# Kernel optimization log

Hardware: AMD Instinct MI355X
Metric: run time of the kernel (lower is better)

## Reference

```python
import jax, jax.numpy as jnp
import numpy as np

TEMP = 0.05
MOMENTUM = 0.2
NUM_SAMPLES = 65536
NUM_FEATURES = 256
BATCH = 512
EPS = 1e-12

def _l2norm(x, axis=-1):
    return x / jnp.sqrt(jnp.sum(x * x, axis=axis, keepdims=True) + EPS)

def setup_inputs() -> dict:
    key = jax.random.key(0)
    k1, k2, k3 = jax.random.split(key, 3)
    inputs = _l2norm(jax.random.normal(k1, (BATCH, NUM_FEATURES), dtype=jnp.float32))
    targets = jax.random.randint(k2, (BATCH,), 0, NUM_SAMPLES, dtype=jnp.int32)
    features = _l2norm(jax.random.normal(k3, (NUM_SAMPLES, NUM_FEATURES), dtype=jnp.float32))
    return {"inputs": inputs, "targets": targets, "features": features}

def reference(inputs, targets, features):
    # ClusterMemory forward (mode='CM'): logits = (inputs @ features.T) / temp
    logits = jnp.matmul(inputs, features.T) / TEMP  # [B, num_samples]

    # CM side-effect: sequential per-sample EMA scatter update of the memory bank
    # features[y] = m*features[y] + (1-m)*x; features[y] /= ||features[y]||
    # Order-dependent over the batch (duplicate targets), so use lax.scan.
    def step(feats, xy):
        x, y = xy
        row = MOMENTUM * feats[y] + (1.0 - MOMENTUM) * x
        row = row / jnp.sqrt(jnp.sum(row * row) + EPS)
        return feats.at[y].set(row), None

    new_features, _ = jax.lax.scan(step, features, (inputs, targets))
    return logits, new_features
```

## Files before the change

### kernel.cpp

```cpp
#include <hip/hip_runtime.h>
#include <hip/hip_bf16.h>

#define NSAMP   65536
#define NFEAT   256
#define BATCHSZ 512
#define LOGITS_ELEMS ((size_t)BATCHSZ * NSAMP)

typedef __attribute__((ext_vector_type(4))) float f32x4;
typedef __attribute__((ext_vector_type(8))) short bf16x8;

#define BM 128
#define BN 128
#define BK 64

#define B_HI_OFF ((size_t)0)
#define B_LO_OFF ((size_t)33554432)
#define A_HI_OFF ((size_t)67108864)
#define A_LO_OFF ((size_t)67371008)
#define WS_NEEDED ((size_t)(67371008 + 262144))
#define CHUNK_BYTES 16384

#define FSLOTS (NSAMP * (NFEAT / 8))
#define ASLOTS (BATCHSZ * (NFEAT / 8))

__device__ inline unsigned short bf16_bits(float x) {
  return __builtin_bit_cast(unsigned short, __float2bfloat16(x));
}

#define GLOAD_LDS16(gp, lp)                                         \
  __builtin_amdgcn_global_load_lds(                                 \
      (const __attribute__((address_space(1))) void*)(gp),          \
      (__attribute__((address_space(3))) void*)(lp), 16, 0, 0)

__global__ __launch_bounds__(256)
void cm_pack_kernel(const float* __restrict__ inputs,
                    const float* __restrict__ features,
                    char* __restrict__ ws,
                    float* __restrict__ newF) {
  const int idx = blockIdx.x * 256 + threadIdx.x;
  const float* g;
  size_t dst_hi, dst_lo;
  if (idx < FSLOTS) {
    const int R = idx >> 5, s5 = idx & 31;
    g = features + (size_t)R * NFEAT + s5 * 8;
    const int p = R >> 7, r = R & 127, ks = s5 >> 3, slot = s5 & 7;
    const size_t off = (size_t)(p * 4 + ks) * CHUNK_BYTES +
                       r * 128 + ((slot * 16) ^ ((r & 7) << 4));
    dst_hi = B_HI_OFF + off;
    dst_lo = B_LO_OFF + off;
    float* o = newF + (size_t)R * NFEAT + s5 * 8;
    *(f32x4*)o       = *(const f32x4*)g;
    *(f32x4*)(o + 4) = *(const f32x4*)(g + 4);
  } else if (idx < FSLOTS + ASLOTS) {
    const int j = idx - FSLOTS;
    const int R = j >> 5, s5 = j & 31;
    g = inputs + (size_t)R * NFEAT + s5 * 8;
    const int p = R >> 7, r = R & 127, ks = s5 >> 3, slot = s5 & 7;
    const size_t off = (size_t)(p * 4 + ks) * CHUNK_BYTES +
                       r * 128 + ((slot * 16) ^ ((r & 7) << 4));
    dst_hi = A_HI_OFF + off;
    dst_lo = A_LO_OFF + off;
  } else {
    return;
  }
  f32x4 v0 = *(const f32x4*)g;
  f32x4 v1 = *(const f32x4*)(g + 4);
  bf16x8 hi, lo;
  #pragma unroll
  for (int e = 0; e < 8; ++e) {
    float x = (e < 4) ? v0[e & 3] : v1[e & 3];
    unsigned short h = bf16_bits(x);
    float hf = __bfloat162float(__builtin_bit_cast(__hip_bfloat16, h));
    hi[e] = (short)h;
    lo[e] = (short)bf16_bits(x - hf);
  }
  *(bf16x8*)(ws + dst_hi) = hi;
  *(bf16x8*)(ws + dst_lo) = lo;
}

__device__ __forceinline__ void mfma_block(const char* smem, int lane,
                                           int m_off, int n_off,
                                           f32x4 acc[4][4]) {
  #pragma unroll
  for (int kc = 0; kc < 2; ++kc) {
    const int kbyte = kc * 64 + ((lane >> 4) << 4);
    const int xr    = (lane & 7) << 4;
    bf16x8 ah[4], al[4], bh[4], bl[4];
    #pragma unroll
    for (int m = 0; m < 4; ++m) {
      const int r   = m_off + m * 16 + (lane & 15);
      const int off = r * 128 + (kbyte ^ xr);
      ah[m] = *(const bf16x8*)(smem + off);
      al[m] = *(const bf16x8*)(smem + CHUNK_BYTES + off);
    }
    #pragma unroll
    for (int n = 0; n < 4; ++n) {
      const int r   = n_off + n * 16 + (lane & 15);
      const int off = r * 128 + (kbyte ^ xr);
      bh[n] = *(const bf16x8*)(smem + 2 * CHUNK_BYTES + off);
      bl[n] = *(const bf16x8*)(smem + 3 * CHUNK_BYTES + off);
    }
    #pragma unroll
    for (int m = 0; m < 4; ++m)
      #pragma unroll
      for (int n = 0; n < 4; ++n) {
        acc[m][n] = __builtin_amdgcn_mfma_f32_16x16x32_bf16(ah[m], bh[n], acc[m][n], 0, 0, 0);
        acc[m][n] = __builtin_amdgcn_mfma_f32_16x16x32_bf16(al[m], bh[n], acc[m][n], 0, 0, 0);
        acc[m][n] = __builtin_amdgcn_mfma_f32_16x16x32_bf16(ah[m], bl[n], acc[m][n], 0, 0, 0);
      }
  }
}

__device__ __forceinline__ void gemm_epilogue(float* logits, f32x4 acc[4][4],
                                              int m_tile, int n_tile,
                                              int m_off, int n_off, int lane) {
  const float scale = 20.0f;
  const int c_col      = n_tile * BN + n_off + (lane & 15);
  const int c_row_base = m_tile * BM + m_off + ((lane >> 4) << 2);
  #pragma unroll
  for (int m = 0; m < 4; ++m) {
    #pragma unroll
    for (int n = 0; n < 4; ++n) {
      f32x4 v = acc[m][n];
      size_t base = (size_t)(c_row_base + m * 16) * NSAMP + (size_t)(c_col + n * 16);
      logits[base]             = v[0] * scale;
      logits[base + NSAMP]     = v[1] * scale;
      logits[base + 2 * NSAMP] = v[2] * scale;
      logits[base + 3 * NSAMP] = v[3] * scale;
    }
  }
}

__global__ __launch_bounds__(256, 2)
void cm_gemm_kernel(const char* __restrict__ ws,
                    float* __restrict__ logits) {
  __shared__ __align__(16) char smem[4 * CHUNK_BYTES];

  const int tid = threadIdx.x;
  const int bid = blockIdx.x;
  const int swz    = (bid & 7) * 256 + (bid >> 3);
  const int m_tile = swz & 3;
  const int n_tile = swz >> 2;

  const int wave  = tid >> 6;
  const int lane  = tid & 63;
  const int m_off = (wave >> 1) * 64;
  const int n_off = (wave & 1) * 64;

  f32x4 acc[4][4];
  #pragma unroll
  for (int m = 0; m < 4; ++m)
    #pragma unroll
    for (int n = 0; n < 4; ++n) {
      acc[m][n][0] = 0.0f; acc[m][n][1] = 0.0f;
      acc[m][n][2] = 0.0f; acc[m][n][3] = 0.0f;
    }

  const size_t a_base = (size_t)(m_tile * 4) * CHUNK_BYTES;
  const size_t b_base = (size_t)(n_tile * 4) * CHUNK_BYTES;

  for (int ks = 0; ks < 4; ++ks) {
    if (ks) __syncthreads();

    const size_t ac = a_base + (size_t)ks * CHUNK_BYTES;
    const size_t bc = b_base + (size_t)ks * CHUNK_BYTES;
    #pragma unroll
    for (int i = 0; i < 4; ++i) {
      const size_t t = (size_t)i * 4096 + (size_t)tid * 16;
      GLOAD_LDS16(ws + A_HI_OFF + ac + t, smem + 0 * CHUNK_BYTES + t);
      GLOAD_LDS16(ws + A_LO_OFF + ac + t, smem + 1 * CHUNK_BYTES + t);
      GLOAD_LDS16(ws + B_HI_OFF + bc + t, smem + 2 * CHUNK_BYTES + t);
      GLOAD_LDS16(ws + B_LO_OFF + bc + t, smem + 3 * CHUNK_BYTES + t);
    }
    __syncthreads();

    mfma_block(smem, lane, m_off, n_off, acc);
  }

  gemm_epilogue(logits, acc, m_tile, n_tile, m_off, n_off, lane);
}

__global__ __launch_bounds__(256, 2)
void cm_gemm_fused_kernel(const float* __restrict__ inputs,
                          const float* __restrict__ features,
                          float* __restrict__ logits,
                          float* __restrict__ newF) {
  __shared__ __align__(16) char smem[4 * CHUNK_BYTES];

  const int tid    = threadIdx.x;
  const int bidx   = blockIdx.x;
  const int m_tile = bidx & 3;
  const int n_tile = bidx >> 2;
  const int bm0    = m_tile * BM;
  const int bn0    = n_tile * BN;

  const int wave  = tid >> 6;
  const int lane  = tid & 63;
  const int m_off = (wave >> 1) * 64;
  const int n_off = (wave & 1) * 64;

  f32x4 acc[4][4];
  #pragma unroll
  for (int m = 0; m < 4; ++m)
    #pragma unroll
    for (int n = 0; n < 4; ++n) {
      acc[m][n][0] = 0.0f; acc[m][n][1] = 0.0f;
      acc[m][n][2] = 0.0f; acc[m][n][3] = 0.0f;
    }

  const int srow = tid >> 3;
  const int slot = tid & 7;

  for (int ks = 0; ks < 4; ++ks) {
    const int k0 = ks * BK;
    if (ks) __syncthreads();

    #pragma unroll
    for (int s = 0; s < 4; ++s) {
      const int row     = srow + s * 32;
      const int byteoff = row * 128 + ((slot * 16) ^ ((row & 7) << 4));
      {
        const float* g = inputs + (size_t)(bm0 + row) * NFEAT + k0 + slot * 8;
        f32x4 v0 = *(const f32x4*)g;
        f32x4 v1 = *(const f32x4*)(g + 4);
        bf16x8 hi, lo;
        #pragma unroll
        for (int e = 0; e < 8; ++e) {
          float x = (e < 4) ? v0[e & 3] : v1[e & 3];
          unsigned short h = bf16_bits(x);
          float hf = __bfloat162float(__builtin_bit_cast(__hip_bfloat16, h));
          hi[e] = (short)h;
          lo[e] = (short)bf16_bits(x - hf);
        }
        *(bf16x8*)(smem + byteoff)               = hi;
        *(bf16x8*)(smem + CHUNK_BYTES + byteoff) = lo;
      }
      {
        const float* g = features + (size_t)(bn0 + row) * NFEAT + k0 + slot * 8;
        f32x4 v0 = *(const f32x4*)g;
        f32x4 v1 = *(const f32x4*)(g + 4);
        bf16x8 hi, lo;
        #pragma unroll
        for (int e = 0; e < 8; ++e) {
          float x = (e < 4) ? v0[e & 3] : v1[e & 3];
          unsigned short h = bf16_bits(x);
          float hf = __bfloat162float(__builtin_bit_cast(__hip_bfloat16, h));
          hi[e] = (short)h;
          lo[e] = (short)bf16_bits(x - hf);
        }
        *(bf16x8*)(smem + 2 * CHUNK_BYTES + byteoff) = hi;
        *(bf16x8*)(smem + 3 * CHUNK_BYTES + byteoff) = lo;
        if (m_tile == 0) {
          float* o = newF + (size_t)(bn0 + row) * NFEAT + k0 + slot * 8;
          *(f32x4*)o       = v0;
          *(f32x4*)(o + 4) = v1;
        }
      }
    }
    __syncthreads();

    mfma_block(smem, lane, m_off, n_off, acc);
  }

  gemm_epilogue(logits, acc, m_tile, n_tile, m_off, n_off, lane);
}

__global__ __launch_bounds__(64)
void cm_update_kernel(const float* __restrict__ inputs,
                      const int* __restrict__ targets,
                      const float* __restrict__ features,
                      float* __restrict__ newF) {
  const int i    = blockIdx.x;
  const int lane = threadIdx.x;
  const int y    = targets[i];

  unsigned long long m[8];
  #pragma unroll
  for (int c = 0; c < 8; ++c)
    m[c] = __ballot(targets[c * 64 + lane] == y);

  int maxj = -1;
  #pragma unroll
  for (int c = 7; c >= 0; --c)
    if (maxj < 0 && m[c]) maxj = c * 64 + 63 - __clzll(m[c]);
  if (maxj != i) return;

  f32x4 row = *(const f32x4*)(features + (size_t)y * NFEAT + lane * 4);
  for (int c = 0; c < 8; ++c) {
    unsigned long long mm = m[c];
    while (mm) {
      const int b = __builtin_ctzll(mm);
      mm &= mm - 1;
      const int j = c * 64 + b;
      f32x4 x = *(const f32x4*)(inputs + (size_t)j * NFEAT + lane * 4);
      row[0] = 0.2f * row[0] + 0.8f * x[0];
      row[1] = 0.2f * row[1] + 0.8f * x[1];
      row[2] = 0.2f * row[2] + 0.8f * x[2];
      row[3] = 0.2f * row[3] + 0.8f * x[3];
      float p = row[0]*row[0] + row[1]*row[1] + row[2]*row[2] + row[3]*row[3];
      #pragma unroll
      for (int off = 32; off >= 1; off >>= 1)
        p += __shfl_xor(p, off);
      const float inv = 1.0f / sqrtf(p + 1e-12f);
      row[0] *= inv; row[1] *= inv; row[2] *= inv; row[3] *= inv;
    }
  }
  *(f32x4*)(newF + (size_t)y * NFEAT + lane * 4) = row;
}

extern "C" void kernel_launch(void* const* d_in, const int* in_sizes, int n_in,
                              void* d_out, int out_size, void* d_ws, size_t ws_size,
                              hipStream_t stream) {
  const float* inputs   = (const float*)d_in[0];
  const int*   targets  = (const int*)d_in[1];
  const float* features = (const float*)d_in[2];
  float* logits = (float*)d_out;
  float* newF   = (float*)d_out + LOGITS_ELEMS;

  const int grid = (NSAMP / BN) * (BATCHSZ / BM);

  if (ws_size >= WS_NEEDED) {
    char* ws = (char*)d_ws;
    const int pack_blocks = (FSLOTS + ASLOTS) / 256;
    cm_pack_kernel<<<pack_blocks, 256, 0, stream>>>(inputs, features, ws, newF);
    cm_gemm_kernel<<<grid, 256, 0, stream>>>(ws, logits);
  } else {
    cm_gemm_fused_kernel<<<grid, 256, 0, stream>>>(inputs, features, logits, newF);
  }

  cm_update_kernel<<<BATCHSZ, 64, 0, stream>>>(inputs, targets, features, newF);
}
```

Before: 312.2 us.

## Double-buffer LDS with 32-wide K stages in packed-workspace GEMM

Repacks the bf16 hi/lo workspace into 8 K-stages of 32 elements (64-byte rows with a 4-way XOR swizzle) instead of 4 stages of 64. The GEMM kernel now double-buffers LDS, issuing the asynchronous global-to-LDS loads for the next stage while MFMAs run on the current one, with a single barrier per stage. The goal is to hide global load latency behind compute at the cost of more barriers and a smaller swizzle that may cause some LDS bank conflicts. The fused kernel only inlines its old MFMA helper and is otherwise unchanged.

```diff
diff --git a/kernel.cpp b/kernel.cpp
--- a/kernel.cpp
+++ b/kernel.cpp
@@ -11,14 +11,14 @@
 
 #define BM 128
 #define BN 128
-#define BK 64
-
+
+#define CHUNK 8192
 #define B_HI_OFF ((size_t)0)
 #define B_LO_OFF ((size_t)33554432)
 #define A_HI_OFF ((size_t)67108864)
 #define A_LO_OFF ((size_t)67371008)
 #define WS_NEEDED ((size_t)(67371008 + 262144))
-#define CHUNK_BYTES 16384
+#define OLDCHUNK 16384
 
 #define FSLOTS (NSAMP * (NFEAT / 8))
 #define ASLOTS (BATCHSZ * (NFEAT / 8))
@@ -43,9 +43,9 @@
   if (idx < FSLOTS) {
     const int R = idx >> 5, s5 = idx & 31;
     g = features + (size_t)R * NFEAT + s5 * 8;
-    const int p = R >> 7, r = R & 127, ks = s5 >> 3, slot = s5 & 7;
-    const size_t off = (size_t)(p * 4 + ks) * CHUNK_BYTES +
-                       r * 128 + ((slot * 16) ^ ((r & 7) << 4));
+    const int p = R >> 7, r = R & 127, s = s5 >> 2, sl = s5 & 3;
+    const size_t off = (size_t)(p * 8 + s) * CHUNK +
+                       r * 64 + ((sl * 16) ^ ((r & 3) << 4));
     dst_hi = B_HI_OFF + off;
     dst_lo = B_LO_OFF + off;
     float* o = newF + (size_t)R * NFEAT + s5 * 8;
@@ -55,9 +55,9 @@
     const int j = idx - FSLOTS;
     const int R = j >> 5, s5 = j & 31;
     g = inputs + (size_t)R * NFEAT + s5 * 8;
-    const int p = R >> 7, r = R & 127, ks = s5 >> 3, slot = s5 & 7;
-    const size_t off = (size_t)(p * 4 + ks) * CHUNK_BYTES +
-                       r * 128 + ((slot * 16) ^ ((r & 7) << 4));
+    const int p = R >> 7, r = R & 127, s = s5 >> 2, sl = s5 & 3;
+    const size_t off = (size_t)(p * 8 + s) * CHUNK +
+                       r * 64 + ((sl * 16) ^ ((r & 3) << 4));
     dst_hi = A_HI_OFF + off;
     dst_lo = A_LO_OFF + off;
   } else {
@@ -76,39 +76,6 @@
   }
   *(bf16x8*)(ws + dst_hi) = hi;
   *(bf16x8*)(ws + dst_lo) = lo;
-}
-
-__device__ __forceinline__ void mfma_block(const char* smem, int lane,
-                                           int m_off, int n_off,
-                                           f32x4 acc[4][4]) {
-  #pragma unroll
-  for (int kc = 0; kc < 2; ++kc) {
-    const int kbyte = kc * 64 + ((lane >> 4) << 4);
-    const int xr    = (lane & 7) << 4;
-    bf16x8 ah[4], al[4], bh[4], bl[4];
-    #pragma unroll
-    for (int m = 0; m < 4; ++m) {
-      const int r   = m_off + m * 16 + (lane & 15);
-      const int off = r * 128 + (kbyte ^ xr);
-      ah[m] = *(const bf16x8*)(smem + off);
-      al[m] = *(const bf16x8*)(smem + CHUNK_BYTES + off);
-    }
-    #pragma unroll
-    for (int n = 0; n < 4; ++n) {
-      const int r   = n_off + n * 16 + (lane & 15);
-      const int off = r * 128 + (kbyte ^ xr);
-      bh[n] = *(const bf16x8*)(smem + 2 * CHUNK_BYTES + off);
-      bl[n] = *(const bf16x8*)(smem + 3 * CHUNK_BYTES + off);
-    }
-    #pragma unroll
-    for (int m = 0; m < 4; ++m)
-      #pragma unroll
-      for (int n = 0; n < 4; ++n) {
-        acc[m][n] = __builtin_amdgcn_mfma_f32_16x16x32_bf16(ah[m], bh[n], acc[m][n], 0, 0, 0);
-        acc[m][n] = __builtin_amdgcn_mfma_f32_16x16x32_bf16(al[m], bh[n], acc[m][n], 0, 0, 0);
-        acc[m][n] = __builtin_amdgcn_mfma_f32_16x16x32_bf16(ah[m], bl[n], acc[m][n], 0, 0, 0);
-      }
-  }
 }
 
 __device__ __forceinline__ void gemm_epilogue(float* logits, f32x4 acc[4][4],
@@ -134,7 +101,7 @@
 __global__ __launch_bounds__(256, 2)
 void cm_gemm_kernel(const char* __restrict__ ws,
                     float* __restrict__ logits) {
-  __shared__ __align__(16) char smem[4 * CHUNK_BYTES];
+  __shared__ __align__(16) char smem[2][4 * CHUNK];
 
   const int tid = threadIdx.x;
   const int bid = blockIdx.x;
@@ -156,26 +123,61 @@
       acc[m][n][2] = 0.0f; acc[m][n][3] = 0.0f;
     }
 
-  const size_t a_base = (size_t)(m_tile * 4) * CHUNK_BYTES;
-  const size_t b_base = (size_t)(n_tile * 4) * CHUNK_BYTES;
-
-  for (int ks = 0; ks < 4; ++ks) {
-    if (ks) __syncthreads();
-
-    const size_t ac = a_base + (size_t)ks * CHUNK_BYTES;
-    const size_t bc = b_base + (size_t)ks * CHUNK_BYTES;
-    #pragma unroll
-    for (int i = 0; i < 4; ++i) {
-      const size_t t = (size_t)i * 4096 + (size_t)tid * 16;
-      GLOAD_LDS16(ws + A_HI_OFF + ac + t, smem + 0 * CHUNK_BYTES + t);
-      GLOAD_LDS16(ws + A_LO_OFF + ac + t, smem + 1 * CHUNK_BYTES + t);
-      GLOAD_LDS16(ws + B_HI_OFF + bc + t, smem + 2 * CHUNK_BYTES + t);
-      GLOAD_LDS16(ws + B_LO_OFF + bc + t, smem + 3 * CHUNK_BYTES + t);
-    }
+  const size_t a_base = (size_t)(m_tile * 8) * CHUNK;
+  const size_t b_base = (size_t)(n_tile * 8) * CHUNK;
+
+  #define STAGE(buf, s)                                                     \
+    do {                                                                    \
+      const size_t ac = a_base + (size_t)(s) * CHUNK;                       \
+      const size_t bc = b_base + (size_t)(s) * CHUNK;                       \
+      _Pragma("unroll")                                                     \
+      for (int i = 0; i < 2; ++i) {                                         \
+        const size_t t = (size_t)i * 4096 + (size_t)tid * 16;               \
+        GLOAD_LDS16(ws + A_HI_OFF + ac + t, &smem[buf][0 * CHUNK + t]);     \
+        GLOAD_LDS16(ws + A_LO_OFF + ac + t, &smem[buf][1 * CHUNK + t]);     \
+        GLOAD_LDS16(ws + B_HI_OFF + bc + t, &smem[buf][2 * CHUNK + t]);     \
+        GLOAD_LDS16(ws + B_LO_OFF + bc + t, &smem[buf][3 * CHUNK + t]);     \
+      }                                                                     \
+    } while (0)
+
+  STAGE(0, 0);
+  __syncthreads();
+
+  #pragma unroll
+  for (int s = 0; s < 8; ++s) {
+    if (s < 7) STAGE((s + 1) & 1, s + 1);
+
+    {
+      const char* sm  = smem[s & 1];
+      const int kbyte = (lane >> 4) << 4;
+      bf16x8 ah[4], al[4], bh[4], bl[4];
+      #pragma unroll
+      for (int m = 0; m < 4; ++m) {
+        const int r   = m_off + m * 16 + (lane & 15);
+        const int off = r * 64 + (kbyte ^ ((r & 3) << 4));
+        ah[m] = *(const bf16x8*)(sm + off);
+        al[m] = *(const bf16x8*)(sm + CHUNK + off);
+      }
+      #pragma unroll
+      for (int n = 0; n < 4; ++n) {
+        const int r   = n_off + n * 16 + (lane & 15);
+        const int off = r * 64 + (kbyte ^ ((r & 3) << 4));
+        bh[n] = *(const bf16x8*)(sm + 2 * CHUNK + off);
+        bl[n] = *(const bf16x8*)(sm + 3 * CHUNK + off);
+      }
+      #pragma unroll
+      for (int m = 0; m < 4; ++m)
+        #pragma unroll
+        for (int n = 0; n < 4; ++n) {
+          acc[m][n] = __builtin_amdgcn_mfma_f32_16x16x32_bf16(ah[m], bh[n], acc[m][n], 0, 0, 0);
+          acc[m][n] = __builtin_amdgcn_mfma_f32_16x16x32_bf16(al[m], bh[n], acc[m][n], 0, 0, 0);
+          acc[m][n] = __builtin_amdgcn_mfma_f32_16x16x32_bf16(ah[m], bl[n], acc[m][n], 0, 0, 0);
+        }
+    }
+
     __syncthreads();
-
-    mfma_block(smem, lane, m_off, n_off, acc);
-  }
+  }
+  #undef STAGE
 
   gemm_epilogue(logits, acc, m_tile, n_tile, m_off, n_off, lane);
 }
@@ -185,7 +187,7 @@
                           const float* __restrict__ features,
                           float* __restrict__ logits,
                           float* __restrict__ newF) {
-  __shared__ __align__(16) char smem[4 * CHUNK_BYTES];
+  __shared__ __align__(16) char smem[4 * OLDCHUNK];
 
   const int tid    = threadIdx.x;
   const int bidx   = blockIdx.x;
@@ -212,7 +214,7 @@
   const int slot = tid & 7;
 
   for (int ks = 0; ks < 4; ++ks) {
-    const int k0 = ks * BK;
+    const int k0 = ks * 64;
     if (ks) __syncthreads();
 
     #pragma unroll
@@ -232,8 +234,8 @@
           hi[e] = (short)h;
           lo[e] = (short)bf16_bits(x - hf);
         }
-        *(bf16x8*)(smem + byteoff)               = hi;
-        *(bf16x8*)(smem + CHUNK_BYTES + byteoff) = lo;
+        *(bf16x8*)(smem + byteoff)            = hi;
+        *(bf16x8*)(smem + OLDCHUNK + byteoff) = lo;
       }
       {
         const float* g = features + (size_t)(bn0 + row) * NFEAT + k0 + slot * 8;
@@ -248,8 +250,8 @@
           hi[e] = (short)h;
           lo[e] = (short)bf16_bits(x - hf);
         }
-        *(bf16x8*)(smem + 2 * CHUNK_BYTES + byteoff) = hi;
-        *(bf16x8*)(smem + 3 * CHUNK_BYTES + byteoff) = lo;
+        *(bf16x8*)(smem + 2 * OLDCHUNK + byteoff) = hi;
+        *(bf16x8*)(smem + 3 * OLDCHUNK + byteoff) = lo;
         if (m_tile == 0) {
           float* o = newF + (size_t)(bn0 + row) * NFEAT + k0 + slot * 8;
           *(f32x4*)o       = v0;
@@ -259,7 +261,34 @@
     }
     __syncthreads();
 
-    mfma_block(smem, lane, m_off, n_off, acc);
+    #pragma unroll
+    for (int kc = 0; kc < 2; ++kc) {
+      const int kbyte = kc * 64 + ((lane >> 4) << 4);
+      const int xr    = (lane & 7) << 4;
+      bf16x8 ah[4], al[4], bh[4], bl[4];
+      #pragma unroll
+      for (int m = 0; m < 4; ++m) {
+        const int r   = m_off + m * 16 + (lane & 15);
+        const int off = r * 128 + (kbyte ^ xr);
+        ah[m] = *(const bf16x8*)(smem + off);
+        al[m] = *(const bf16x8*)(smem + OLDCHUNK + off);
+      }
+      #pragma unroll
+      for (int n = 0; n < 4; ++n) {
+        const int r   = n_off + n * 16 + (lane & 15);
+        const int off = r * 128 + (kbyte ^ xr);
+        bh[n] = *(const bf16x8*)(smem + 2 * OLDCHUNK + off);
+        bl[n] = *(const bf16x8*)(smem + 3 * OLDCHUNK + off);
+      }
+      #pragma unroll
+      for (int m = 0; m < 4; ++m)
+        #pragma unroll
+        for (int n = 0; n < 4; ++n) {
+          acc[m][n] = __builtin_amdgcn_mfma_f32_16x16x32_bf16(ah[m], bh[n], acc[m][n], 0, 0, 0);
+          acc[m][n] = __builtin_amdgcn_mfma_f32_16x16x32_bf16(al[m], bh[n], acc[m][n], 0, 0, 0);
+          acc[m][n] = __builtin_amdgcn_mfma_f32_16x16x32_bf16(ah[m], bl[n], acc[m][n], 0, 0, 0);
+        }
+    }
   }
 
   gemm_epilogue(logits, acc, m_tile, n_tile, m_off, n_off, lane);
```

After: 310.8 us. No clear change (-0.4%).
